# Performance work log

Measured on AMD Instinct MI355X. Metric: run time of the kernel, lower is better.

## Reference

```python
import jax, jax.numpy as jnp
import numpy as np

N, E, G = 25600, 409600, 128   # nodes, edges, graphs
IN, H, C = 200, 4, 64          # raw feat dim, heads, hidden_channels
IN2 = 2 * IN                   # after NaN-mask concat
BN_EPS = 1e-5

def _glorot(key, shape):
    lim = float(np.sqrt(6.0 / (shape[0] + shape[-1])))
    return jax.random.uniform(key, shape, jnp.float32, -lim, lim)

def setup_inputs():
    key = jax.random.key(0)
    k = iter(jax.random.split(key, 40))
    inp = {
        "x": jax.random.normal(next(k), (N, IN), jnp.float32),
        "edge_index": jax.random.randint(next(k), (2, E), 0, N, jnp.int32),
        "edge_attr": jax.random.normal(next(k), (E, 1), jnp.float32),
        "batch": jnp.repeat(jnp.arange(G, dtype=jnp.int32), N // G),
    }
    dims = [(IN2, H, C), (H * C, H, C), (H * C, 1, C)]
    for i, (din, h, c) in enumerate(dims):
        inp[f"W{i}"] = _glorot(next(k), (din, h * c))
        inp[f"as{i}"] = _glorot(next(k), (h, c))
        inp[f"ad{i}"] = _glorot(next(k), (h, c))
        inp[f"We{i}"] = _glorot(next(k), (1, h * c))
        inp[f"ae{i}"] = _glorot(next(k), (h, c))
        inp[f"b{i}"] = jnp.zeros((h * c,), jnp.float32)
    inp["bn_g"] = jnp.ones((H * C,), jnp.float32)
    inp["bn_b"] = jnp.zeros((H * C,), jnp.float32)
    inp["bn_m"] = jnp.zeros((H * C,), jnp.float32)
    inp["bn_v"] = jnp.ones((H * C,), jnp.float32)
    inp["cw1"] = _glorot(next(k), (C, C))
    inp["cb1"] = jnp.zeros((C,), jnp.float32)
    inp["cw2"] = _glorot(next(k), (C, 2))
    inp["cb2"] = jnp.zeros((2,), jnp.float32)
    return inp

def _gat(x, src, dst, ea, W, att_s, att_d, We, att_e, b, heads, ch):
    """PyG GATConv (edge_dim=1, add_self_loops=True, fill_value='mean', concat=True)."""
    n = x.shape[0]
    # self-loop edge_attr = mean of incoming edge_attr per destination node
    cnt = jax.ops.segment_sum(jnp.ones((ea.shape[0], 1), ea.dtype), dst, n)
    loop_ea = jax.ops.segment_sum(ea, dst, n) / jnp.maximum(cnt, 1.0)
    idx = jnp.arange(n, dtype=src.dtype)
    src = jnp.concatenate([src, idx])
    dst = jnp.concatenate([dst, idx])
    ea = jnp.concatenate([ea, loop_ea], axis=0)
    h = (x @ W).reshape(n, heads, ch)                      # [N,H,C]
    a_s = jnp.einsum('nhc,hc->nh', h, att_s)
    a_d = jnp.einsum('nhc,hc->nh', h, att_d)
    a_e = jnp.einsum('ehc,hc->eh', (ea @ We).reshape(-1, heads, ch), att_e)
    alpha = jax.nn.leaky_relu(a_s[src] + a_d[dst] + a_e, 0.2)   # [E',H]
    # segment softmax over destination neighborhoods
    m = jax.ops.segment_max(alpha, dst, n)
    ex = jnp.exp(alpha - m[dst])
    z = jax.ops.segment_sum(ex, dst, n)
    alpha = ex / (z[dst] + 1e-16)
    out = jax.ops.segment_sum(h[src] * alpha[:, :, None], dst, n)  # [N,H,C]
    return out.reshape(n, heads * ch) + b

def reference(x, edge_index, edge_attr, batch,
              W0, as0, ad0, We0, ae0, b0,
              W1, as1, ad1, We1, ae1, b1,
              W2, as2, ad2, We2, ae2, b2,
              bn_g, bn_b, bn_m, bn_v, cw1, cb1, cw2, cb2):
    nan_mask = jnp.isnan(x).astype(x.dtype)
    x = jnp.concatenate([jnp.nan_to_num(x), nan_mask], axis=-1)   # [N, 2*IN]
    edge_attr = jnp.nan_to_num(edge_attr)
    src, dst = edge_index[0], edge_index[1]
    for (W, a_s, a_d, We, a_e, b) in [(W0, as0, ad0, We0, ae0, b0),
                                      (W1, as1, ad1, We1, ae1, b1)]:
        x = _gat(x, src, dst, edge_attr, W, a_s, a_d, We, a_e, b, H, C)
        x = (x - bn_m) / jnp.sqrt(bn_v + BN_EPS) * bn_g + bn_b    # eval-mode BN
        x = jax.nn.relu(x)                                        # dropout = identity (eval)
    x = _gat(x, src, dst, edge_attr, W2, as2, ad2, We2, ae2, b2, 1, C)
    # global mean pool over graphs
    cnt = jax.ops.segment_sum(jnp.ones((x.shape[0], 1), x.dtype), batch, G)
    g = jax.ops.segment_sum(x, batch, G) / jnp.maximum(cnt, 1.0)  # [G, C]
    hdn = jax.nn.gelu(g @ cw1 + cb1, approximate=False)
    return hdn @ cw2 + cb2                                        # [G, 2]
```

## Files before the change

kernel.cpp:

```cpp
#include <hip/hip_runtime.h>
#include <hip/hip_bf16.h>

static const int kN  = 25600;
static const int kE  = 409600;
static const int kG  = 128;
static const int kNPG = 200;
static const int kIN = 200;
static const int kIN2 = 400;
static const int kK0 = 448;
static const int kMD = 64;
#define BN_EPS_ 1e-5f

typedef __attribute__((ext_vector_type(8))) short short8;
typedef __attribute__((ext_vector_type(4))) ushort us4;
typedef __attribute__((ext_vector_type(4))) float f32x4;

__device__ __forceinline__ float bu(ushort u) {
  union { float f; unsigned u32; } x; x.u32 = ((unsigned)u) << 16; return x.f;
}
__device__ __forceinline__ ushort f2u(float v) {
  __hip_bfloat16 t = __float2bfloat16(v);
  return *(ushort*)&t;
}
__device__ __forceinline__ float wredSum(float v) {
#pragma unroll
  for (int off = 1; off < 64; off <<= 1) v += __shfl_xor(v, off, 64);
  return v;
}
__device__ __forceinline__ float lrelu(float a) { return (a > 0.f) ? a : 0.2f * a; }

#define GLOAD16(g, l) __builtin_amdgcn_global_load_lds( \
    (const __attribute__((address_space(1))) unsigned int*)(g), \
    (__attribute__((address_space(3))) unsigned int*)(l), 16, 0, 0)

__global__ void k_pre(const float* __restrict__ x, ushort* __restrict__ x2,
                      const float* __restrict__ W0, ushort* __restrict__ Wt0,
                      const float* __restrict__ W1, ushort* __restrict__ Wt1,
                      const float* __restrict__ W2, ushort* __restrict__ Wt2,
                      const float* __restrict__ We0, const float* __restrict__ ae0,
                      const float* __restrict__ We1, const float* __restrict__ ae1,
                      const float* __restrict__ We2, const float* __restrict__ ae2,
                      float* __restrict__ wed,
                      const int* __restrict__ ei, const float* __restrict__ ea,
                      int2* __restrict__ epk, int* __restrict__ deg) {
  int b = blockIdx.x, tid = threadIdx.x;
  if (b < 5000) {
    int i4 = (b * 256 + tid) * 4;
    int n = i4 / kIN, j = i4 - n * kIN;
    float4 v = *(const float4*)&x[i4];
    ushort o0[4], o1[4];
    float vv[4] = {v.x, v.y, v.z, v.w};
#pragma unroll
    for (int q = 0; q < 4; q++) {
      bool bad = (vv[q] != vv[q]);
      o0[q] = f2u(bad ? 0.f : vv[q]);
      o1[q] = f2u(bad ? 1.f : 0.f);
    }
    *(us4*)&x2[(size_t)n * kK0 + j] = *(us4*)o0;
    *(us4*)&x2[(size_t)n * kK0 + kIN + j] = *(us4*)o1;
    return;
  }
  int pb = b - 5000;
  if (pb >= 2323) {
    int idx = (pb - 2323) * 256 + tid;
    short8 z = {0, 0, 0, 0, 0, 0, 0, 0};
    if (idx < 153600) {
      int row = idx / 6, c = idx - row * 6;
      *(short8*)&x2[(size_t)row * kK0 + kIN2 + c * 8] = z;
    } else {
      int j = idx - 153600;
      if (j < 1536) {
        int row = j / 6, c = j - row * 6;
        *(short8*)&Wt0[(size_t)row * kK0 + kIN2 + c * 8] = z;
      }
    }
    return;
  }
  if (pb >= 723) {
    int e = (pb - 723) * 256 + tid;
    int d = ei[kE + e];
    int s = ei[e];
    float v = ea[e];
    if (v != v) v = 0.f;
    int slot = atomicAdd(&deg[d], 1);
    if (slot < kMD) {
      int2 rec; rec.x = s; rec.y = __float_as_int(v);
      epk[(size_t)d * kMD + slot] = rec;
    }
    return;
  }
  if (pb >= 720) {
    int l = pb - 720;
    const float* We = (l == 0) ? We0 : (l == 1) ? We1 : We2;
    const float* ae = (l == 0) ? ae0 : (l == 1) ? ae1 : ae2;
    int n = (l == 2) ? 64 : 256;
    float v = (tid < n) ? We[tid] * ae[tid] : 0.f;
    v = wredSum(v);
    if ((tid & 63) == 0 && tid < n) wed[l * 4 + (tid >> 6)] = v;
    return;
  }
  int i = pb * 256 + tid;
  if (i < 102400) {
    int n = i / kIN2, k = i - n * kIN2;
    Wt0[(size_t)n * kK0 + k] = f2u(W0[(size_t)k * 256 + n]);
  } else if (i < 102400 + 65536) {
    int j = i - 102400;
    int n = j >> 8, k = j & 255;
    Wt1[(size_t)n * 256 + k] = f2u(W1[(size_t)k * 256 + n]);
  } else {
    int j = i - 102400 - 65536;
    int n = j >> 8, k = j & 255;
    Wt2[(size_t)n * 256 + k] = f2u(W2[(size_t)k * 64 + n]);
  }
}

template <int BN, int MT>
__global__ __launch_bounds__(256) void k_gemm_f(const ushort* __restrict__ A,
                                                const ushort* __restrict__ Bt,
                                                ushort* __restrict__ C,
                                                const float* __restrict__ as_g,
                                                const float* __restrict__ ad_g,
                                                float* __restrict__ a_sg,
                                                float* __restrict__ a_dg, int K) {
  constexpr int MI = (BN == 256) ? (MT / 16) : 1;
  constexpr int H = (BN == 256) ? 4 : 1;
  __shared__ ushort As[MT * 64];
  __shared__ ushort Bs[BN * 64];
  int tid = threadIdx.x;
  int lane = tid & 63, w = tid >> 6;
  int l15 = lane & 15, l4 = lane >> 4;
  int row0 = blockIdx.y * MT;
  int wr = (BN == 256) ? 0 : (w * 16);
  int wc = (BN == 256) ? (w * 64) : 0;
  f32x4 acc[MI][4] = {};
  int srow = lane >> 3;
  int schunk = lane & 7;

  for (int kt = 0; kt < K; kt += 64) {
    __syncthreads();
#pragma unroll
    for (int i = 0; i < MT / 32; i++) {
      int ra = w * (MT / 4) + i * 8;
      int r = ra + srow;
      GLOAD16(&A[(size_t)(row0 + r) * K + kt + ((schunk ^ (r & 7)) * 8)],
              &As[ra * 64]);
    }
#pragma unroll
    for (int i = 0; i < BN / 32; i++) {
      int rb = w * (BN / 4) + i * 8;
      int r = rb + srow;
      GLOAD16(&Bt[(size_t)r * K + kt + ((schunk ^ (r & 7)) * 8)],
              &Bs[rb * 64]);
    }
    __syncthreads();
#pragma unroll
    for (int kk = 0; kk < 2; kk++) {
      short8 af[MI], bf[4];
#pragma unroll
      for (int mi = 0; mi < MI; mi++) {
        int r = wr + mi * 16 + l15;
        af[mi] = *(const short8*)&As[r * 64 + ((kk * 32 + l4 * 8) ^ ((r & 7) * 8))];
      }
#pragma unroll
      for (int ni = 0; ni < 4; ni++) {
        int r = wc + ni * 16 + l15;
        bf[ni] = *(const short8*)&Bs[r * 64 + ((kk * 32 + l4 * 8) ^ ((r & 7) * 8))];
      }
#pragma unroll
      for (int mi = 0; mi < MI; mi++)
#pragma unroll
        for (int ni = 0; ni < 4; ni++)
          acc[mi][ni] = __builtin_amdgcn_mfma_f32_16x16x32_bf16(af[mi], bf[ni],
                                                                acc[mi][ni], 0, 0, 0);
    }
  }
#pragma unroll
  for (int mi = 0; mi < MI; mi++) {
    int rbase = row0 + wr + mi * 16 + l4 * 4;
#pragma unroll
    for (int ni = 0; ni < 4; ni++) {
      int col = wc + ni * 16 + l15;
#pragma unroll
      for (int r = 0; r < 4; r++)
        C[(size_t)(rbase + r) * BN + col] = f2u(acc[mi][ni][r]);
    }
  }
  float asv[4], adv[4];
#pragma unroll
  for (int ni = 0; ni < 4; ni++) {
    asv[ni] = as_g[wc + ni * 16 + l15];
    adv[ni] = ad_g[wc + ni * 16 + l15];
  }
  int hh = (BN == 256) ? w : 0;
#pragma unroll
  for (int mi = 0; mi < MI; mi++) {
#pragma unroll
    for (int r = 0; r < 4; r++) {
      float ps = 0.f, pd = 0.f;
#pragma unroll
      for (int ni = 0; ni < 4; ni++) {
        ps += acc[mi][ni][r] * asv[ni];
        pd += acc[mi][ni][r] * adv[ni];
      }
#pragma unroll
      for (int off = 1; off < 16; off <<= 1) {
        ps += __shfl_xor(ps, off, 64);
        pd += __shfl_xor(pd, off, 64);
      }
      if (l15 == 0) {
        int row = row0 + wr + mi * 16 + l4 * 4 + r;
        a_sg[row * H + hh] = ps;
        a_dg[row * H + hh] = pd;
      }
    }
  }
}

__global__ __launch_bounds__(256) void k_agg4(
    const ushort* __restrict__ hbuf, const int2* __restrict__ epk,
    const int* __restrict__ deg, const float* __restrict__ a_s,
    const float* __restrict__ a_d, const float* __restrict__ wed,
    const float* __restrict__ bias, const float* __restrict__ bng,
    const float* __restrict__ bnb, const float* __restrict__ bnm,
    const float* __restrict__ bnv, ushort* __restrict__ xout) {
  __shared__ float lds_w[4][kMD][4];
  __shared__ int   lds_s[4][kMD];
  __shared__ float lds_m[4][4][2];
  int tid = threadIdx.x;
  int w = tid >> 6, lane = tid & 63;
  int d = blockIdx.x * 4 + w;
  const int2* rp = &epk[(size_t)d * kMD];
  int dgt = deg[d];
  int dg = min(dgt, kMD);

  int h1 = lane & 3, slot0 = lane >> 2;
  float adh1 = a_d[d * 4 + h1];
  float wdh1 = wed[h1];
  float szp = 0.f, seap = 0.f;
  for (int t = 0; t < dg; t += 16) {
    int slot = t + slot0;
    float wv = 0.f, ev = 0.f;
    if (slot < dg) {
      int2 rec = rp[slot];
      ev = __int_as_float(rec.y);
      float asv = a_s[rec.x * 4 + h1];
      wv = __expf(lrelu(asv + adh1 + ev * wdh1));
      lds_w[w][slot][h1] = wv;
      if (h1 == 0) lds_s[w][slot] = rec.x;
    }
    szp += wv;
    seap += (h1 == 0) ? ev : 0.f;
  }
#pragma unroll
  for (int off = 4; off < 64; off <<= 1) {
    szp  += __shfl_xor(szp, off, 64);
    seap += __shfl_xor(seap, off, 64);
  }
  float sea = __shfl(seap, lane & 0x3C, 64);
  float lea = sea / fmaxf((float)dgt, 1.f);
  float selfw1 = __expf(lrelu(a_s[d * 4 + h1] + adh1 + lea * wdh1));
  float szh = szp + selfw1;
  if (slot0 == 0) {
    lds_m[w][h1][0] = 1.f / (szh + 1e-16f);
    lds_m[w][h1][1] = selfw1;
  }

  int h2 = lane >> 4;
  int c0 = lane * 4;
  ushort4 vself = *(const ushort4*)&hbuf[(size_t)d * 256 + c0];
  float a0 = 0.f, a1 = 0.f, a2 = 0.f, a3 = 0.f;
  int k = 0;
  for (; k + 16 <= dg; k += 16) {
    int s16[16]; float w16[16];
#pragma unroll
    for (int j = 0; j < 16; j++) {
      s16[j] = lds_s[w][k + j];
      w16[j] = lds_w[w][k + j][h2];
    }
    ushort4 v16[16];
#pragma unroll
    for (int j = 0; j < 16; j++)
      v16[j] = *(const ushort4*)&hbuf[(size_t)s16[j] * 256 + c0];
#pragma unroll
    for (int j = 0; j < 16; j++) {
      a0 += w16[j] * bu(v16[j].x); a1 += w16[j] * bu(v16[j].y);
      a2 += w16[j] * bu(v16[j].z); a3 += w16[j] * bu(v16[j].w);
    }
  }
  for (; k + 8 <= dg; k += 8) {
    int s8[8]; float w8[8];
#pragma unroll
    for (int j = 0; j < 8; j++) {
      s8[j] = lds_s[w][k + j];
      w8[j] = lds_w[w][k + j][h2];
    }
    ushort4 v8[8];
#pragma unroll
    for (int j = 0; j < 8; j++)
      v8[j] = *(const ushort4*)&hbuf[(size_t)s8[j] * 256 + c0];
#pragma unroll
    for (int j = 0; j < 8; j++) {
      a0 += w8[j] * bu(v8[j].x); a1 += w8[j] * bu(v8[j].y);
      a2 += w8[j] * bu(v8[j].z); a3 += w8[j] * bu(v8[j].w);
    }
  }
  for (; k < dg; k++) {
    int s0 = lds_s[w][k];
    float w0 = lds_w[w][k][h2];
    ushort4 v0 = *(const ushort4*)&hbuf[(size_t)s0 * 256 + c0];
    a0 += w0 * bu(v0.x); a1 += w0 * bu(v0.y);
    a2 += w0 * bu(v0.z); a3 += w0 * bu(v0.w);
  }
  float winv = lds_m[w][h2][0];
  float sw   = lds_m[w][h2][1];
  a0 += sw * bu(vself.x); a1 += sw * bu(vself.y);
  a2 += sw * bu(vself.z); a3 += sw * bu(vself.w);

  float4 bi = *(const float4*)&bias[c0];
  a0 = a0 * winv + bi.x; a1 = a1 * winv + bi.y;
  a2 = a2 * winv + bi.z; a3 = a3 * winv + bi.w;
  float4 g4 = *(const float4*)&bng[c0], b4 = *(const float4*)&bnb[c0];
  float4 m4 = *(const float4*)&bnm[c0], v4 = *(const float4*)&bnv[c0];
  a0 = fmaxf((a0 - m4.x) * rsqrtf(v4.x + BN_EPS_) * g4.x + b4.x, 0.f);
  a1 = fmaxf((a1 - m4.y) * rsqrtf(v4.y + BN_EPS_) * g4.y + b4.y, 0.f);
  a2 = fmaxf((a2 - m4.z) * rsqrtf(v4.z + BN_EPS_) * g4.z + b4.z, 0.f);
  a3 = fmaxf((a3 - m4.w) * rsqrtf(v4.w + BN_EPS_) * g4.w + b4.w, 0.f);
  ushort4 o = make_ushort4(f2u(a0), f2u(a1), f2u(a2), f2u(a3));
  *(ushort4*)&xout[(size_t)d * 256 + c0] = o;
}

__global__ __launch_bounds__(256) void k_agg1(
    const ushort* __restrict__ hbuf, const int2* __restrict__ epk,
    const int* __restrict__ deg, const float* __restrict__ a_s,
    const float* __restrict__ a_d, const float* __restrict__ wed,
    float* __restrict__ gsum) {
  __shared__ float lds_w[4][kMD];
  __shared__ int   lds_s[4][kMD];
  __shared__ float part[4][64];
  int tid = threadIdx.x;
  int w = tid >> 6, lane = tid & 63;
  int d = blockIdx.x * 4 + w;
  const int2* rp = &epk[(size_t)d * kMD];
  int dgt = deg[d];
  int dg = min(dgt, kMD);
  float adh = a_d[d];
  float wdh = wed[0];

  float wv = 0.f, ev = 0.f;
  if (lane < dg) {
    int2 rec = rp[lane];
    ev = __int_as_float(rec.y);
    wv = __expf(lrelu(a_s[rec.x] + adh + ev * wdh));
    lds_w[w][lane] = wv;
    lds_s[w][lane] = rec.x;
  }
  float szp = wv, seap = ev;
#pragma unroll
  for (int off = 1; off < 64; off <<= 1) {
    szp  += __shfl_xor(szp, off, 64);
    seap += __shfl_xor(seap, off, 64);
  }
  float lea = seap / fmaxf((float)dgt, 1.f);
  float selfw = __expf(lrelu(a_s[d] + adh + lea * wdh));
  float winv = 1.f / (szp + selfw + 1e-16f);

  float vselff = bu(hbuf[(size_t)d * 64 + lane]);
  float acc = 0.f;
  int k = 0;
  for (; k + 16 <= dg; k += 16) {
    int s16[16]; float w16[16];
#pragma unroll
    for (int j = 0; j < 16; j++) {
      s16[j] = lds_s[w][k + j];
      w16[j] = lds_w[w][k + j];
    }
    ushort v16[16];
#pragma unroll
    for (int j = 0; j < 16; j++) v16[j] = hbuf[(size_t)s16[j] * 64 + lane];
#pragma unroll
    for (int j = 0; j < 16; j++) acc += w16[j] * bu(v16[j]);
  }
  for (; k + 8 <= dg; k += 8) {
    int s8[8]; float w8[8];
#pragma unroll
    for (int j = 0; j < 8; j++) {
      s8[j] = lds_s[w][k + j];
      w8[j] = lds_w[w][k + j];
    }
    ushort v8[8];
#pragma unroll
    for (int j = 0; j < 8; j++) v8[j] = hbuf[(size_t)s8[j] * 64 + lane];
#pragma unroll
    for (int j = 0; j < 8; j++) acc += w8[j] * bu(v8[j]);
  }
  for (; k < dg; k++) {
    acc += lds_w[w][k] * bu(hbuf[(size_t)lds_s[w][k] * 64 + lane]);
  }
  acc += selfw * vselff;
  acc = acc * winv;

  part[w][lane] = acc;
  __syncthreads();
  if (w == 0) {
    float s = (part[0][lane] + part[1][lane]) + (part[2][lane] + part[3][lane]);
    int g = (blockIdx.x * 4) / kNPG;
    atomicAdd(&gsum[g * 64 + lane], s);
  }
}

__global__ void k_head(const float* __restrict__ gsum, const float* __restrict__ bias,
                       const float* __restrict__ cw1, const float* __restrict__ cb1,
                       const float* __restrict__ cw2, const float* __restrict__ cb2,
                       float* __restrict__ out) {
  __shared__ float gb[64], hb[64];
  int g = blockIdx.x, c = threadIdx.x;
  gb[c] = gsum[g * 64 + c] * (1.f / kNPG) + bias[c];
  __syncthreads();
  float s = cb1[c];
#pragma unroll 8
  for (int i = 0; i < 64; i++) s += gb[i] * cw1[i * 64 + c];
  s = 0.5f * s * (1.f + erff(s * 0.70710678118654752f));
  hb[c] = s;
  __syncthreads();
  if (c < 2) {
    float o = cb2[c];
    for (int i = 0; i < 64; i++) o += hb[i] * cw2[i * 2 + c];
    out[g * 2 + c] = o;
  }
}


extern "C" void kernel_launch(void* const* d_in, const int* in_sizes, int n_in,
                              void* d_out, int out_size, void* d_ws, size_t ws_size,
                              hipStream_t stream) {
  (void)in_sizes; (void)n_in; (void)out_size; (void)ws_size;
  const float* x  = (const float*)d_in[0];
  const int* ei   = (const int*)d_in[1];
  const float* ea = (const float*)d_in[2];
  const float *W[3], *as_[3], *ad_[3], *We[3], *ae[3], *bi[3];
  for (int l = 0; l < 3; l++) {
    W[l]   = (const float*)d_in[4 + l * 6 + 0];
    as_[l] = (const float*)d_in[4 + l * 6 + 1];
    ad_[l] = (const float*)d_in[4 + l * 6 + 2];
    We[l]  = (const float*)d_in[4 + l * 6 + 3];
    ae[l]  = (const float*)d_in[4 + l * 6 + 4];
    bi[l]  = (const float*)d_in[4 + l * 6 + 5];
  }
  const float* bng = (const float*)d_in[22];
  const float* bnb = (const float*)d_in[23];
  const float* bnm = (const float*)d_in[24];
  const float* bnv = (const float*)d_in[25];
  const float* cw1 = (const float*)d_in[26];
  const float* cb1 = (const float*)d_in[27];
  const float* cw2 = (const float*)d_in[28];
  const float* cb2 = (const float*)d_in[29];

  char* p = (char*)d_ws;
  auto alloc = [&](size_t bytes) -> void* {
    void* r = (void*)p;
    p += (bytes + 255) & ~(size_t)255;
    return r;
  };
  ushort* x2b   = (ushort*)alloc((size_t)kN * kK0 * 2);
  ushort* hbufb = (ushort*)alloc((size_t)kN * 256 * 2);
  ushort* xbA   = (ushort*)alloc((size_t)kN * 256 * 2);
  ushort* xbB   = (ushort*)alloc((size_t)kN * 256 * 2);
  ushort* Wt0   = (ushort*)alloc((size_t)kK0 * 256 * 2);
  ushort* Wt1   = (ushort*)alloc((size_t)256 * 256 * 2);
  ushort* Wt2   = (ushort*)alloc((size_t)256 * 64 * 2);
  float* a_s    = (float*)alloc((size_t)kN * 4 * 4);
  float* a_d    = (float*)alloc((size_t)kN * 4 * 4);
  int2* epk     = (int2*)alloc((size_t)kN * kMD * 8);
  float* wed    = (float*)alloc(256);
  int* deg      = (int*)alloc((size_t)kN * 4);
  float* gsum   = (float*)alloc((size_t)kG * 64 * 4);

  hipMemsetAsync(deg, 0, (size_t)kN * 4 + (size_t)kG * 64 * 4, stream);
  k_pre<<<5000 + 2929, 256, 0, stream>>>(
      x, x2b, W[0], Wt0, W[1], Wt1, W[2], Wt2, We[0], ae[0], We[1], ae[1],
      We[2], ae[2], wed, ei, ea, epk, deg);
  dim3 gg64m(1, kN / 64);
  k_gemm_f<256, 64><<<gg64m, 256, 0, stream>>>(x2b, Wt0, hbufb, as_[0], ad_[0],
                                               a_s, a_d, kK0);
  k_agg4<<<kN / 4, 256, 0, stream>>>(hbufb, epk, deg, a_s, a_d,
                                     &wed[0], bi[0], bng, bnb, bnm, bnv, xbA);
  k_gemm_f<256, 64><<<gg64m, 256, 0, stream>>>(xbA, Wt1, hbufb, as_[1], ad_[1],
                                               a_s, a_d, 256);
  k_agg4<<<kN / 4, 256, 0, stream>>>(hbufb, epk, deg, a_s, a_d,
                                     &wed[4], bi[1], bng, bnb, bnm, bnv, xbB);
  dim3 gg64(1, kN / 64);
  k_gemm_f<64, 64><<<gg64, 256, 0, stream>>>(xbB, Wt2, hbufb, as_[2], ad_[2],
                                             a_s, a_d, 256);
  k_agg1<<<kN / 4, 256, 0, stream>>>(hbufb, epk, deg, a_s, a_d, &wed[8], gsum);
  k_head<<<kG, 64, 0, stream>>>(gsum, bi[2], cw1, cb1, cw2, cb2, (float*)d_out);
}
```

Baseline: 292.8 us.

## Store hidden features head-major and split aggregation per head

The GEMM output, the attention logits and the intermediate activations move from node-major [N,256] to head-major [4][N,64] layout, and the following GEMMs read A in that layout. The 4-head aggregation kernel now gives each wavefront one (node, head) pair, with a grid of N blocks. Blocks are interleaved so that every head's 64-column slab is gathered by concurrent blocks, which should raise cache locality for the random neighbour gathers (a 3.2MB slab instead of a 13MB table). In exchange, edge records and logits are re-read once per head, and each lane loads a single 2-byte value instead of an 8-byte vector.

```diff
diff --git a/kernel.cpp b/kernel.cpp
--- a/kernel.cpp
+++ b/kernel.cpp
@@ -114,7 +114,7 @@
   }
 }
 
-template <int BN, int MT>
+template <int BN, int MT, bool AHM>
 __global__ __launch_bounds__(256) void k_gemm_f(const ushort* __restrict__ A,
                                                 const ushort* __restrict__ Bt,
                                                 ushort* __restrict__ C,
@@ -123,7 +123,6 @@
                                                 float* __restrict__ a_sg,
                                                 float* __restrict__ a_dg, int K) {
   constexpr int MI = (BN == 256) ? (MT / 16) : 1;
-  constexpr int H = (BN == 256) ? 4 : 1;
   __shared__ ushort As[MT * 64];
   __shared__ ushort Bs[BN * 64];
   int tid = threadIdx.x;
@@ -142,8 +141,11 @@
     for (int i = 0; i < MT / 32; i++) {
       int ra = w * (MT / 4) + i * 8;
       int r = ra + srow;
-      GLOAD16(&A[(size_t)(row0 + r) * K + kt + ((schunk ^ (r & 7)) * 8)],
-              &As[ra * 64]);
+      const ushort* ap = AHM
+          ? &A[(size_t)(kt >> 6) * ((size_t)kN * 64) + (size_t)(row0 + r) * 64 +
+               ((schunk ^ (r & 7)) * 8)]
+          : &A[(size_t)(row0 + r) * K + kt + ((schunk ^ (r & 7)) * 8)];
+      GLOAD16(ap, &As[ra * 64]);
     }
 #pragma unroll
     for (int i = 0; i < BN / 32; i++) {
@@ -181,8 +183,12 @@
     for (int ni = 0; ni < 4; ni++) {
       int col = wc + ni * 16 + l15;
 #pragma unroll
-      for (int r = 0; r < 4; r++)
-        C[(size_t)(rbase + r) * BN + col] = f2u(acc[mi][ni][r]);
+      for (int r = 0; r < 4; r++) {
+        size_t caddr = (BN == 256)
+            ? ((size_t)w * ((size_t)kN * 64) + (size_t)(rbase + r) * 64 + (col & 63))
+            : ((size_t)(rbase + r) * BN + col);
+        C[caddr] = f2u(acc[mi][ni][r]);
+      }
     }
   }
   float asv[4], adv[4];
@@ -191,7 +197,6 @@
     asv[ni] = as_g[wc + ni * 16 + l15];
     adv[ni] = ad_g[wc + ni * 16 + l15];
   }
-  int hh = (BN == 256) ? w : 0;
 #pragma unroll
   for (int mi = 0; mi < MI; mi++) {
 #pragma unroll
@@ -209,8 +214,9 @@
       }
       if (l15 == 0) {
         int row = row0 + wr + mi * 16 + l4 * 4 + r;
-        a_sg[row * H + hh] = ps;
-        a_dg[row * H + hh] = pd;
+        size_t aaddr = (BN == 256) ? ((size_t)w * kN + row) : (size_t)row;
+        a_sg[aaddr] = ps;
+        a_dg[aaddr] = pd;
       }
     }
   }
@@ -223,110 +229,78 @@
     const float* __restrict__ bias, const float* __restrict__ bng,
     const float* __restrict__ bnb, const float* __restrict__ bnm,
     const float* __restrict__ bnv, ushort* __restrict__ xout) {
-  __shared__ float lds_w[4][kMD][4];
+  __shared__ float lds_w[4][kMD];
   __shared__ int   lds_s[4][kMD];
-  __shared__ float lds_m[4][4][2];
   int tid = threadIdx.x;
   int w = tid >> 6, lane = tid & 63;
-  int d = blockIdx.x * 4 + w;
+  int bid = blockIdx.x;
+  int r8 = bid & 7;
+  int head = r8 >> 1;
+  int dgroup = (r8 & 1) * 3200 + (bid >> 3);
+  int d = dgroup * 4 + w;
+  const ushort* hb = hbuf + (size_t)head * kN * 64;
+  const float* asg = a_s + (size_t)head * kN;
   const int2* rp = &epk[(size_t)d * kMD];
   int dgt = deg[d];
   int dg = min(dgt, kMD);
-
-  int h1 = lane & 3, slot0 = lane >> 2;
-  float adh1 = a_d[d * 4 + h1];
-  float wdh1 = wed[h1];
-  float szp = 0.f, seap = 0.f;
-  for (int t = 0; t < dg; t += 16) {
-    int slot = t + slot0;
-    float wv = 0.f, ev = 0.f;
-    if (slot < dg) {
-      int2 rec = rp[slot];
-      ev = __int_as_float(rec.y);
-      float asv = a_s[rec.x * 4 + h1];
-      wv = __expf(lrelu(asv + adh1 + ev * wdh1));
-      lds_w[w][slot][h1] = wv;
-      if (h1 == 0) lds_s[w][slot] = rec.x;
-    }
-    szp += wv;
-    seap += (h1 == 0) ? ev : 0.f;
-  }
-#pragma unroll
-  for (int off = 4; off < 64; off <<= 1) {
+  float adh = a_d[(size_t)head * kN + d];
+  float wdh = wed[head];
+
+  float wv = 0.f, ev = 0.f;
+  if (lane < dg) {
+    int2 rec = rp[lane];
+    ev = __int_as_float(rec.y);
+    wv = __expf(lrelu(asg[rec.x] + adh + ev * wdh));
+    lds_w[w][lane] = wv;
+    lds_s[w][lane] = rec.x;
+  }
+  float szp = wv, seap = ev;
+#pragma unroll
+  for (int off = 1; off < 64; off <<= 1) {
     szp  += __shfl_xor(szp, off, 64);
     seap += __shfl_xor(seap, off, 64);
   }
-  float sea = __shfl(seap, lane & 0x3C, 64);
-  float lea = sea / fmaxf((float)dgt, 1.f);
-  float selfw1 = __expf(lrelu(a_s[d * 4 + h1] + adh1 + lea * wdh1));
-  float szh = szp + selfw1;
-  if (slot0 == 0) {
-    lds_m[w][h1][0] = 1.f / (szh + 1e-16f);
-    lds_m[w][h1][1] = selfw1;
-  }
-
-  int h2 = lane >> 4;
-  int c0 = lane * 4;
-  ushort4 vself = *(const ushort4*)&hbuf[(size_t)d * 256 + c0];
-  float a0 = 0.f, a1 = 0.f, a2 = 0.f, a3 = 0.f;
+  float lea = seap / fmaxf((float)dgt, 1.f);
+  float selfw = __expf(lrelu(asg[d] + adh + lea * wdh));
+  float winv = 1.f / (szp + selfw + 1e-16f);
+
+  float vself = bu(hb[(size_t)d * 64 + lane]);
+  float acc = 0.f;
   int k = 0;
   for (; k + 16 <= dg; k += 16) {
     int s16[16]; float w16[16];
 #pragma unroll
     for (int j = 0; j < 16; j++) {
       s16[j] = lds_s[w][k + j];
-      w16[j] = lds_w[w][k + j][h2];
-    }
-    ushort4 v16[16];
-#pragma unroll
-    for (int j = 0; j < 16; j++)
-      v16[j] = *(const ushort4*)&hbuf[(size_t)s16[j] * 256 + c0];
-#pragma unroll
-    for (int j = 0; j < 16; j++) {
-      a0 += w16[j] * bu(v16[j].x); a1 += w16[j] * bu(v16[j].y);
-      a2 += w16[j] * bu(v16[j].z); a3 += w16[j] * bu(v16[j].w);
-    }
+      w16[j] = lds_w[w][k + j];
+    }
+    ushort v16[16];
+#pragma unroll
+    for (int j = 0; j < 16; j++) v16[j] = hb[(size_t)s16[j] * 64 + lane];
+#pragma unroll
+    for (int j = 0; j < 16; j++) acc += w16[j] * bu(v16[j]);
   }
   for (; k + 8 <= dg; k += 8) {
     int s8[8]; float w8[8];
 #pragma unroll
     for (int j = 0; j < 8; j++) {
       s8[j] = lds_s[w][k + j];
-      w8[j] = lds_w[w][k + j][h2];
-    }
-    ushort4 v8[8];
-#pragma unroll
-    for (int j = 0; j < 8; j++)
-      v8[j] = *(const ushort4*)&hbuf[(size_t)s8[j] * 256 + c0];
-#pragma unroll
-    for (int j = 0; j < 8; j++) {
-      a0 += w8[j] * bu(v8[j].x); a1 += w8[j] * bu(v8[j].y);
-      a2 += w8[j] * bu(v8[j].z); a3 += w8[j] * bu(v8[j].w);
-    }
-  }
-  for (; k < dg; k++) {
-    int s0 = lds_s[w][k];
-    float w0 = lds_w[w][k][h2];
-    ushort4 v0 = *(const ushort4*)&hbuf[(size_t)s0 * 256 + c0];
-    a0 += w0 * bu(v0.x); a1 += w0 * bu(v0.y);
-    a2 += w0 * bu(v0.z); a3 += w0 * bu(v0.w);
-  }
-  float winv = lds_m[w][h2][0];
-  float sw   = lds_m[w][h2][1];
-  a0 += sw * bu(vself.x); a1 += sw * bu(vself.y);
-  a2 += sw * bu(vself.z); a3 += sw * bu(vself.w);
-
-  float4 bi = *(const float4*)&bias[c0];
-  a0 = a0 * winv + bi.x; a1 = a1 * winv + bi.y;
-  a2 = a2 * winv + bi.z; a3 = a3 * winv + bi.w;
-  float4 g4 = *(const float4*)&bng[c0], b4 = *(const float4*)&bnb[c0];
-  float4 m4 = *(const float4*)&bnm[c0], v4 = *(const float4*)&bnv[c0];
-  a0 = fmaxf((a0 - m4.x) * rsqrtf(v4.x + BN_EPS_) * g4.x + b4.x, 0.f);
-  a1 = fmaxf((a1 - m4.y) * rsqrtf(v4.y + BN_EPS_) * g4.y + b4.y, 0.f);
-  a2 = fmaxf((a2 - m4.z) * rsqrtf(v4.z + BN_EPS_) * g4.z + b4.z, 0.f);
-  a3 = fmaxf((a3 - m4.w) * rsqrtf(v4.w + BN_EPS_) * g4.w + b4.w, 0.f);
-  ushort4 o = make_ushort4(f2u(a0), f2u(a1), f2u(a2), f2u(a3));
-  *(ushort4*)&xout[(size_t)d * 256 + c0] = o;
+      w8[j] = lds_w[w][k + j];
+    }
+    ushort v8[8];
+#pragma unroll
+    for (int j = 0; j < 8; j++) v8[j] = hb[(size_t)s8[j] * 64 + lane];
+#pragma unroll
+    for (int j = 0; j < 8; j++) acc += w8[j] * bu(v8[j]);
+  }
+  for (; k < dg; k++)
+    acc += lds_w[w][k] * bu(hb[(size_t)lds_s[w][k] * 64 + lane]);
+  acc += selfw * vself;
+
+  int c = head * 64 + lane;
+  acc = acc * winv + bias[c];
+  acc = fmaxf((acc - bnm[c]) * rsqrtf(bnv[c] + BN_EPS_) * bng[c] + bnb[c], 0.f);
+  xout[(size_t)head * kN * 64 + (size_t)d * 64 + lane] = f2u(acc);
 }
 
 __global__ __launch_bounds__(256) void k_agg1(
@@ -480,17 +454,17 @@
       x, x2b, W[0], Wt0, W[1], Wt1, W[2], Wt2, We[0], ae[0], We[1], ae[1],
       We[2], ae[2], wed, ei, ea, epk, deg);
   dim3 gg64m(1, kN / 64);
-  k_gemm_f<256, 64><<<gg64m, 256, 0, stream>>>(x2b, Wt0, hbufb, as_[0], ad_[0],
-                                               a_s, a_d, kK0);
-  k_agg4<<<kN / 4, 256, 0, stream>>>(hbufb, epk, deg, a_s, a_d,
-                                     &wed[0], bi[0], bng, bnb, bnm, bnv, xbA);
-  k_gemm_f<256, 64><<<gg64m, 256, 0, stream>>>(xbA, Wt1, hbufb, as_[1], ad_[1],
-                                               a_s, a_d, 256);
-  k_agg4<<<kN / 4, 256, 0, stream>>>(hbufb, epk, deg, a_s, a_d,
-                                     &wed[4], bi[1], bng, bnb, bnm, bnv, xbB);
+  k_gemm_f<256, 64, false><<<gg64m, 256, 0, stream>>>(
+      x2b, Wt0, hbufb, as_[0], ad_[0], a_s, a_d, kK0);
+  k_agg4<<<kN, 256, 0, stream>>>(hbufb, epk, deg, a_s, a_d,
+                                 &wed[0], bi[0], bng, bnb, bnm, bnv, xbA);
+  k_gemm_f<256, 64, true><<<gg64m, 256, 0, stream>>>(
+      xbA, Wt1, hbufb, as_[1], ad_[1], a_s, a_d, 256);
+  k_agg4<<<kN, 256, 0, stream>>>(hbufb, epk, deg, a_s, a_d,
+                                 &wed[4], bi[1], bng, bnb, bnm, bnv, xbB);
   dim3 gg64(1, kN / 64);
-  k_gemm_f<64, 64><<<gg64, 256, 0, stream>>>(xbB, Wt2, hbufb, as_[2], ad_[2],
-                                             a_s, a_d, 256);
+  k_gemm_f<64, 64, true><<<gg64, 256, 0, stream>>>(
+      xbB, Wt2, hbufb, as_[2], ad_[2], a_s, a_d, 256);
   k_agg1<<<kN / 4, 256, 0, stream>>>(hbufb, epk, deg, a_s, a_d, &wed[8], gsum);
   k_head<<<kG, 64, 0, stream>>>(gsum, bi[2], cw1, cb1, cw2, cb2, (float*)d_out);
 }
```

Result: slower. 330.4 us (+12.8%).
